# Kernel tuning notes

Measured on AMD Instinct MI355X. Metric: run time of the kernel, lower is better.

The kernel has to match this reference:

```python
import jax, jax.numpy as jnp
import numpy as np

N = 131072      # total nodes
B = 16          # graphs in batch (num_segments)
C = 128         # in_channels
K = 16          # n_super_nodes
TAU = 1.0
PRUNING_THRESHOLD = 0.01
SPARSITY_WEIGHT = 0.01
TEMPORAL_W = 0.1 * 5
COLLAPSE_W = 2.0
EPS = 1e-9


def setup_inputs() -> dict:
    key = jax.random.key(0)
    ks = jax.random.split(key, 8)
    x = jax.random.normal(ks[0], (N, C), dtype=jnp.float32)
    batch = jnp.sort(jax.random.randint(ks[1], (N,), 0, B)).astype(jnp.int64)
    pos = jax.random.normal(ks[2], (N, 2), dtype=jnp.float32)
    # Gumbel noise for gumbel_softmax (sampled once, passed as input for determinism)
    gumbel = jax.random.gumbel(ks[3], (N, K), dtype=jnp.float32)
    # assign_mlp params: Linear(C,C) -> ReLU -> Linear(C,K)
    W1 = jax.random.normal(ks[4], (C, C), dtype=jnp.float32) / np.sqrt(C)
    b1 = jnp.zeros((C,), dtype=jnp.float32)
    W2 = jax.random.normal(ks[5], (K, C), dtype=jnp.float32) / np.sqrt(C)
    b2 = jnp.zeros((K,), dtype=jnp.float32)
    scaling = jnp.asarray(10.0, dtype=jnp.float32)
    active_mask = jnp.ones((K,), dtype=jnp.float32)  # buffer, starts all-active
    return {"x": x, "batch": batch, "pos": pos, "gumbel": gumbel,
            "W1": W1, "b1": b1, "W2": W2, "b2": b2,
            "scaling": scaling, "active_mask": active_mask}


def reference(x, batch, pos, gumbel, W1, b1, W2, b2, scaling, active_mask):
    # --- assignment logits: MLP * scaling (eval mode, prev_assignments=None) ---
    h = jax.nn.relu(x @ W1.T + b1)            # [N, C]
    logits = (h @ W2.T + b2) * scaling        # [N, K]
    # eval-path masking: masked_fill(mask == 0, -1e9)
    masked_logits = jnp.where(active_mask[None, :] == 0.0, -1e9, logits)
    # gumbel_softmax (soft, hard=False)
    s = jax.nn.softmax((masked_logits + gumbel) / TAU, axis=-1)   # [N, K]

    avg_s = jnp.mean(s, axis=0)               # [K]

    # --- losses ---
    entropy = -jnp.mean(jnp.sum(s * jnp.log(s + EPS), axis=1))
    uniform_p = 1.0 / K
    diversity = jnp.sum(uniform_p * jnp.log(uniform_p / (avg_s + EPS)))
    pruning = jnp.mean(jnp.abs(avg_s * (1.0 - active_mask)))
    sparsity = (jnp.sum(active_mask) / K) * SPARSITY_WEIGHT
    temporal = jnp.asarray(0.0, jnp.float32)  # prev_assignments is None
    # collapse-prevention / balance bodies are truncated upstream; faithful proxies
    collapse = jnp.sum((avg_s - uniform_p) ** 2) * COLLAPSE_W
    balance = jnp.std(avg_s)
    spatial = jnp.asarray(0.0, jnp.float32)

    # --- pooled features: out[b,k,c] = sum_{n in graph b} s[n,k] * x[n,c] ---
    weighted = x[:, None, :] * s[:, :, None]                  # [N, K, C]
    out = jax.ops.segment_sum(weighted, batch, num_segments=B)  # [B, K, C]

    # --- super-node positions ---
    w_pos = pos[:, None, :] * s[:, :, None]                    # [N, K, 2]
    sum_s_pos = jax.ops.segment_sum(w_pos, batch, num_segments=B)  # [B, K, 2]
    sum_s = jax.ops.segment_sum(s, batch, num_segments=B)[..., None] + EPS  # [B, K, 1]
    mu = sum_s_pos / sum_s                                     # [B, K, 2]

    # --- separation loss: pairwise repulsion between super-node centers ---
    dist_sq = jnp.sum((mu[:, :, None, :] - mu[:, None, :, :]) ** 2, axis=-1)  # [B,K,K]
    eye = jnp.eye(K, dtype=mu.dtype)[None]
    repulsion = 1.0 / (dist_sq + 1.0)
    separation = jnp.sum(repulsion * (1.0 - eye)) / (K * (K - 1))

    losses = jnp.stack([entropy, diversity, spatial, pruning, sparsity,
                        temporal * TEMPORAL_W, collapse, balance, separation])
    return out, s, mu, losses
```

## Files before the change

### kernel.cpp

```cpp
#include <hip/hip_runtime.h>
#include <hip/hip_bf16.h>
#include <math.h>

#define NN 131072
#define BSEG 16
#define CCH 128
#define KK 16
#define EPSF 1e-9f
#define XST 136

#define OFF_S   32768
#define OFF_MU  2129920
#define OFF_L   2130432

#define REDC_BASE 1024
#define REDC_STRIDE 1024
#define NRED 64
#define ST_BASE (REDC_BASE + NRED * REDC_STRIDE)
#define NST 4
#define ST_SZ (BSEG * KK * CCH)

typedef __bf16 bf16x8 __attribute__((ext_vector_type(8)));
typedef float  f32x4  __attribute__((ext_vector_type(4)));
typedef float  f32x16 __attribute__((ext_vector_type(16)));

__device__ __forceinline__ int load_batch(const void* bptr, int n, int is64) {
    if (is64) return (int)((const long long*)bptr)[n];
    return ((const int*)bptr)[n];
}

__device__ __forceinline__ float wave_sum(float v) {
#pragma unroll
    for (int o = 32; o > 0; o >>= 1) v += __shfl_xor(v, o, 64);
    return v;
}

__device__ __forceinline__ bf16x8 pack8(float4 a, float4 b) {
    bf16x8 v;
    v[0] = (__bf16)a.x; v[1] = (__bf16)a.y; v[2] = (__bf16)a.z; v[3] = (__bf16)a.w;
    v[4] = (__bf16)b.x; v[5] = (__bf16)b.y; v[6] = (__bf16)b.z; v[7] = (__bf16)b.w;
    return v;
}

__global__ void k_zero(float* __restrict__ ws, const int* __restrict__ b32) {
    int i = blockIdx.x * 256 + threadIdx.x;
    ws[REDC_BASE + i] = 0.0f;
    if (i == 0) ws[0] = (b32[NN - 1] == 0) ? 1.0f : 0.0f;
}

__global__ __launch_bounds__(256, 2) void k_fused(
    const float* __restrict__ x, const void* __restrict__ batch,
    const float* __restrict__ pos, const float* __restrict__ gumbel,
    const float* __restrict__ W1, const float* __restrict__ b1,
    const float* __restrict__ W2, const float* __restrict__ b2,
    const float* __restrict__ scaling, const float* __restrict__ active_mask,
    float* __restrict__ s_out, float* __restrict__ ws)
{
    __shared__ __align__(16) __bf16 x_lds[128 * XST];
    __shared__ __align__(16) __bf16 h_lds[128 * XST];
    __shared__ __align__(16) __bf16 sT[16 * XST];
    __shared__ float2 pos_lds[128];
    __shared__ int bsegs[128];

    const int tid  = threadIdx.x;
    const int lane = tid & 63;
    const int wv   = tid >> 6;
    const int n0   = blockIdx.x * 128;
    const int is64 = (int)ws[0];

    float* rc  = ws + REDC_BASE + (size_t)(blockIdx.x & (NRED - 1)) * REDC_STRIDE;
    float* stg = ws + ST_BASE   + (size_t)(blockIdx.x & (NST  - 1)) * ST_SZ;

    if (tid < 128) {
        bsegs[tid] = load_batch(batch, n0 + tid, is64);
        pos_lds[tid] = ((const float2*)pos)[n0 + tid];
    }
    {
        const float4* xg = (const float4*)(x + (size_t)n0 * CCH);
#pragma unroll
        for (int i = 0; i < 8; i++) {
            int p = i * 256 + tid;
            float4 a = xg[2 * p], b = xg[2 * p + 1];
            *(bf16x8*)&x_lds[(p >> 4) * XST + (p & 15) * 8] = pack8(a, b);
        }
    }
    __syncthreads();

    {
        bf16x8 bfr[8];
        const float* wrow = W1 + (size_t)(wv * 32 + (lane & 31)) * CCH + (lane >> 5) * 8;
#pragma unroll
        for (int ks = 0; ks < 8; ks++) {
            float4 u = *(const float4*)(wrow + ks * 16);
            float4 v = *(const float4*)(wrow + ks * 16 + 4);
            bfr[ks] = pack8(u, v);
        }
        f32x16 acc[4];
#pragma unroll
        for (int mt = 0; mt < 4; mt++)
#pragma unroll
            for (int r = 0; r < 16; r++) acc[mt][r] = 0.0f;

#pragma unroll
        for (int ks = 0; ks < 8; ks++) {
#pragma unroll
            for (int mt = 0; mt < 4; mt++) {
                bf16x8 a = *(bf16x8*)&x_lds[(size_t)(mt * 32 + (lane & 31)) * XST + ks * 16 + (lane >> 5) * 8];
                acc[mt] = __builtin_amdgcn_mfma_f32_32x32x16_bf16(a, bfr[ks], acc[mt], 0, 0, 0);
            }
        }
        const float b1j = b1[wv * 32 + (lane & 31)];
#pragma unroll
        for (int mt = 0; mt < 4; mt++)
#pragma unroll
            for (int r = 0; r < 16; r++) {
                int node = mt * 32 + (r & 3) + 8 * (r >> 2) + 4 * (lane >> 5);
                h_lds[(size_t)node * XST + wv * 32 + (lane & 31)] = (__bf16)fmaxf(acc[mt][r] + b1j, 0.0f);
            }
    }
    __syncthreads();

    {
        const int g  = lane >> 4;
        const int kq = lane & 15;
        const int bf = bsegs[0], bl = bsegs[127];

        float gu[2][4];
#pragma unroll
        for (int t = 0; t < 2; t++)
#pragma unroll
            for (int r = 0; r < 4; r++) {
                int node = (wv * 2 + t) * 16 + g * 4 + r;
                gu[t][r] = gumbel[(size_t)(n0 + node) * KK + kq];
            }
        const float b2k = b2[kq];
        const float amk = active_mask[kq];
        const float sc  = scaling[0];

        f32x4 acc2[2];
#pragma unroll
        for (int t = 0; t < 2; t++)
#pragma unroll
            for (int r = 0; r < 4; r++) acc2[t][r] = 0.0f;

#pragma unroll
        for (int ks = 0; ks < 4; ks++) {
            const float* w2row = W2 + (size_t)kq * CCH + ks * 32 + g * 8;
            float4 u = *(const float4*)w2row;
            float4 v4 = *(const float4*)(w2row + 4);
            bf16x8 bwf = pack8(u, v4);
#pragma unroll
            for (int t = 0; t < 2; t++) {
                bf16x8 a = *(bf16x8*)&h_lds[(size_t)((wv * 2 + t) * 16 + kq) * XST + ks * 32 + g * 8];
                acc2[t] = __builtin_amdgcn_mfma_f32_16x16x32_bf16(a, bwf, acc2[t], 0, 0, 0);
            }
        }

        float saccA = 0.f, pxA = 0.f, pyA = 0.f;
        float saccB = 0.f, pxB = 0.f, pyB = 0.f;
        float entacc = 0.f;
        const bool dual = (bf != bl);

#pragma unroll
        for (int t = 0; t < 2; t++) {
#pragma unroll
            for (int r = 0; r < 4; r++) {
                const int node = (wv * 2 + t) * 16 + g * 4 + r;
                float v = (acc2[t][r] + b2k) * sc;
                if (amk == 0.0f) v = -1e9f;
                v += gu[t][r];
                float m = v;
#pragma unroll
                for (int o = 1; o < 16; o <<= 1) m = fmaxf(m, __shfl_xor(m, o, 64));
                float e = expf(v - m);
                float ssum = e;
#pragma unroll
                for (int o = 1; o < 16; o <<= 1) ssum += __shfl_xor(ssum, o, 64);
                float s = e / ssum;

                s_out[(size_t)(n0 + node) * KK + kq] = s;
                sT[kq * XST + node] = (__bf16)s;

                float tt = s * logf(s + EPSF);
#pragma unroll
                for (int o = 1; o < 16; o <<= 1) tt += __shfl_xor(tt, o, 64);
                entacc += tt;

                const float2 pp = pos_lds[node];
                const float w0 = (bsegs[node] == bf) ? 1.0f : 0.0f;
                const float sA = s * w0;
                saccA += sA; pxA += sA * pp.x; pyA += sA * pp.y;
                if (dual) {
                    const float sB = s - sA;
                    saccB += sB; pxB += sB * pp.x; pyB += sB * pp.y;
                }
            }
        }

        saccA += __shfl_xor(saccA, 16, 64); saccA += __shfl_xor(saccA, 32, 64);
        pxA   += __shfl_xor(pxA,   16, 64); pxA   += __shfl_xor(pxA,   32, 64);
        pyA   += __shfl_xor(pyA,   16, 64); pyA   += __shfl_xor(pyA,   32, 64);
        if (lane < 16) {
            atomicAdd(&rc[bf * 16 + lane], saccA);
            atomicAdd(&rc[256 + bf * 32 + 2 * lane],     pxA);
            atomicAdd(&rc[256 + bf * 32 + 2 * lane + 1], pyA);
        }
        if (dual) {
            saccB += __shfl_xor(saccB, 16, 64); saccB += __shfl_xor(saccB, 32, 64);
            pxB   += __shfl_xor(pxB,   16, 64); pxB   += __shfl_xor(pxB,   32, 64);
            pyB   += __shfl_xor(pyB,   16, 64); pyB   += __shfl_xor(pyB,   32, 64);
            if (lane < 16) {
                atomicAdd(&rc[bl * 16 + lane], saccB);
                atomicAdd(&rc[256 + bl * 32 + 2 * lane],     pxB);
                atomicAdd(&rc[256 + bl * 32 + 2 * lane + 1], pyB);
            }
        }
        float entw = wave_sum(entacc);
        if (lane == 0) atomicAdd(&rc[768], entw * 0.0625f);
    }
    __syncthreads();

    {
        const int bfirst = bsegs[0], blast = bsegs[127];
        for (int seg = bfirst; seg <= blast; seg++) {
            const bool masked = (bfirst != blast);
            f32x4 pacc[2];
#pragma unroll
            for (int t = 0; t < 2; t++)
#pragma unroll
                for (int r = 0; r < 4; r++) pacc[t][r] = 0.0f;

#pragma unroll
            for (int ks = 0; ks < 4; ks++) {
                bf16x8 a = *(bf16x8*)&sT[(size_t)(lane & 15) * XST + ks * 32 + (lane >> 4) * 8];
                if (masked) {
#pragma unroll
                    for (int i = 0; i < 8; i++) {
                        int nd = ks * 32 + (lane >> 4) * 8 + i;
                        if (bsegs[nd] != seg) a[i] = (__bf16)0.0f;
                    }
                }
#pragma unroll
                for (int t = 0; t < 2; t++) {
                    int ct = wv * 2 + t;
                    bf16x8 bx;
#pragma unroll
                    for (int i = 0; i < 8; i++)
                        bx[i] = x_lds[(size_t)(ks * 32 + (lane >> 4) * 8 + i) * XST + ct * 16 + (lane & 15)];
                    pacc[t] = __builtin_amdgcn_mfma_f32_16x16x32_bf16(a, bx, pacc[t], 0, 0, 0);
                }
            }
#pragma unroll
            for (int t = 0; t < 2; t++) {
                int c = (wv * 2 + t) * 16 + (lane & 15);
#pragma unroll
                for (int r = 0; r < 4; r++) {
                    int k = (lane >> 4) * 4 + r;
                    atomicAdd(&stg[((size_t)seg * KK + k) * CCH + c], pacc[t][r]);
                }
            }
        }
    }
}

__global__ __launch_bounds__(256) void k_tail(
    const float* __restrict__ ws, const float* __restrict__ active_mask,
    float* __restrict__ out, float* __restrict__ mu_out, float* __restrict__ losses)
{
    const int tid = threadIdx.x;

    if (blockIdx.x < 32) {
        int i = blockIdx.x * 256 + tid;
        const float4* s0 = (const float4*)(ws + ST_BASE);
        const float4* s1 = (const float4*)(ws + ST_BASE + ST_SZ);
        const float4* s2 = (const float4*)(ws + ST_BASE + 2 * ST_SZ);
        const float4* s3 = (const float4*)(ws + ST_BASE + 3 * ST_SZ);
        float4 a = s0[i], b = s1[i], c = s2[i], d = s3[i];
        float4 r;
        r.x = (a.x + b.x) + (c.x + d.x);
        r.y = (a.y + b.y) + (c.y + d.y);
        r.z = (a.z + b.z) + (c.z + d.z);
        r.w = (a.w + b.w) + (c.w + d.w);
        ((float4*)out)[i] = r;
        return;
    }

    __shared__ float lsum[256];
    __shared__ float lpos[512];
    __shared__ float lent[1];
    __shared__ float smu[512];
    __shared__ float savg[16];
    __shared__ float red[256];

    for (int a = tid; a < 769; a += 256) {
        float acc = 0.0f;
#pragma unroll 8
        for (int c = 0; c < NRED; c++) acc += ws[REDC_BASE + c * REDC_STRIDE + a];
        if (a < 256) lsum[a] = acc;
        else if (a < 768) lpos[a - 256] = acc;
        else lent[0] = acc;
    }
    __syncthreads();

    if (tid < 16) {
        float a = 0.0f;
#pragma unroll
        for (int b = 0; b < 16; b++) a += lsum[b * 16 + tid];
        savg[tid] = a / (float)NN;
    }
    for (int i = tid; i < 512; i += 256) {
        int sk = i >> 1;
        float v = lpos[i] / (lsum[sk] + EPSF);
        smu[i] = v;
        mu_out[i] = v;
    }
    __syncthreads();

    float rep = 0.0f;
    for (int t = tid; t < 4096; t += 256) {
        int b = t >> 8, i = (t >> 4) & 15, j = t & 15;
        if (i != j) {
            float dx = smu[b * 32 + i * 2]     - smu[b * 32 + j * 2];
            float dy = smu[b * 32 + i * 2 + 1] - smu[b * 32 + j * 2 + 1];
            rep += 1.0f / (dx * dx + dy * dy + 1.0f);
        }
    }
    red[tid] = rep;
    __syncthreads();
    for (int st = 128; st > 0; st >>= 1) {
        if (tid < st) red[tid] += red[tid + st];
        __syncthreads();
    }

    if (tid == 0) {
        const float p = 1.0f / 16.0f;
        float separation = red[0] / (float)(16 * 15);
        float entropy = -lent[0] / (float)NN;
        float diversity = 0.f, pruning = 0.f, amsum = 0.f, collapse = 0.f, mean = 0.f;
        for (int k = 0; k < 16; k++) {
            float a = savg[k];
            diversity += p * logf(p / (a + EPSF));
            pruning += fabsf(a * (1.0f - active_mask[k]));
            amsum += active_mask[k];
            collapse += (a - p) * (a - p);
            mean += a;
        }
        pruning /= 16.0f;
        mean /= 16.0f;
        float var = 0.f;
        for (int k = 0; k < 16; k++) { float d = savg[k] - mean; var += d * d; }
        float balance = sqrtf(var / 16.0f);
        float sparsity = (amsum / 16.0f) * 0.01f;
        collapse *= 2.0f;
        losses[0] = entropy;   losses[1] = diversity; losses[2] = 0.0f;
        losses[3] = pruning;   losses[4] = sparsity;  losses[5] = 0.0f;
        losses[6] = collapse;  losses[7] = balance;   losses[8] = separation;
    }
}

extern "C" void kernel_launch(void* const* d_in, const int* in_sizes, int n_in,
                              void* d_out, int out_size, void* d_ws, size_t ws_size,
                              hipStream_t stream) {
    const float* x       = (const float*)d_in[0];
    const void*  batch   = d_in[1];
    const float* pos     = (const float*)d_in[2];
    const float* gumbel  = (const float*)d_in[3];
    const float* W1      = (const float*)d_in[4];
    const float* b1      = (const float*)d_in[5];
    const float* W2      = (const float*)d_in[6];
    const float* b2      = (const float*)d_in[7];
    const float* scaling = (const float*)d_in[8];
    const float* am      = (const float*)d_in[9];

    float* out      = (float*)d_out;
    float* s_sec    = out + OFF_S;
    float* mu_sec   = out + OFF_MU;
    float* loss_sec = out + OFF_L;
    float* wsf      = (float*)d_ws;

    k_zero<<<768, 256, 0, stream>>>(wsf, (const int*)batch);
    k_fused<<<NN / 128, 256, 0, stream>>>(x, batch, pos, gumbel, W1, b1, W2, b2,
                                          scaling, am, s_sec, wsf);
    k_tail<<<33, 256, 0, stream>>>(wsf, am, out, mu_sec, loss_sec);
}
```

Measured before the change: 160.8 us.

## Swap GEMM1 warp partition to node rows and drop post-GEMM block barrier

The first MLP layer is repartitioned so each wave owns 32 node rows and all 128 output channels, rather than 32 output channels over all nodes. W1 fragments are now reloaded from global memory (cache) and packed inside the k-loop instead of being preloaded. Because each wave writes only its own rows of h, the __syncthreads after the h store is replaced by a local LDS wait plus a scheduling barrier. This assumes the next stage reads only rows produced by the same wave. The trade is 4x more W1 global loads and pack conversions per wave.

```diff
diff --git a/kernel.cpp b/kernel.cpp
--- a/kernel.cpp
+++ b/kernel.cpp
@@ -87,38 +87,39 @@
     __syncthreads();
 
     {
-        bf16x8 bfr[8];
-        const float* wrow = W1 + (size_t)(wv * 32 + (lane & 31)) * CCH + (lane >> 5) * 8;
-#pragma unroll
+        float b1j[4];
+#pragma unroll
+        for (int ct = 0; ct < 4; ct++) b1j[ct] = b1[ct * 32 + (lane & 31)];
+
+        f32x16 acc[4];
+#pragma unroll
+        for (int ct = 0; ct < 4; ct++)
+#pragma unroll
+            for (int r = 0; r < 16; r++) acc[ct][r] = 0.0f;
+
+        const int arow = wv * 32 + (lane & 31);
+        const int koff = (lane >> 5) * 8;
+#pragma unroll 2
         for (int ks = 0; ks < 8; ks++) {
-            float4 u = *(const float4*)(wrow + ks * 16);
-            float4 v = *(const float4*)(wrow + ks * 16 + 4);
-            bfr[ks] = pack8(u, v);
-        }
-        f32x16 acc[4];
-#pragma unroll
-        for (int mt = 0; mt < 4; mt++)
-#pragma unroll
-            for (int r = 0; r < 16; r++) acc[mt][r] = 0.0f;
-
-#pragma unroll
-        for (int ks = 0; ks < 8; ks++) {
-#pragma unroll
-            for (int mt = 0; mt < 4; mt++) {
-                bf16x8 a = *(bf16x8*)&x_lds[(size_t)(mt * 32 + (lane & 31)) * XST + ks * 16 + (lane >> 5) * 8];
-                acc[mt] = __builtin_amdgcn_mfma_f32_32x32x16_bf16(a, bfr[ks], acc[mt], 0, 0, 0);
-            }
-        }
-        const float b1j = b1[wv * 32 + (lane & 31)];
-#pragma unroll
-        for (int mt = 0; mt < 4; mt++)
+            bf16x8 a = *(bf16x8*)&x_lds[(size_t)arow * XST + ks * 16 + koff];
+#pragma unroll
+            for (int ct = 0; ct < 4; ct++) {
+                const float* wrow = W1 + (size_t)(ct * 32 + (lane & 31)) * CCH + ks * 16 + koff;
+                float4 u = *(const float4*)wrow;
+                float4 v = *(const float4*)(wrow + 4);
+                acc[ct] = __builtin_amdgcn_mfma_f32_32x32x16_bf16(a, pack8(u, v), acc[ct], 0, 0, 0);
+            }
+        }
+#pragma unroll
+        for (int ct = 0; ct < 4; ct++)
 #pragma unroll
             for (int r = 0; r < 16; r++) {
-                int node = mt * 32 + (r & 3) + 8 * (r >> 2) + 4 * (lane >> 5);
-                h_lds[(size_t)node * XST + wv * 32 + (lane & 31)] = (__bf16)fmaxf(acc[mt][r] + b1j, 0.0f);
-            }
-    }
-    __syncthreads();
+                int node = wv * 32 + (r & 3) + 8 * (r >> 2) + 4 * (lane >> 5);
+                h_lds[(size_t)node * XST + ct * 32 + (lane & 31)] = (__bf16)fmaxf(acc[ct][r] + b1j[ct], 0.0f);
+            }
+    }
+    asm volatile("s_waitcnt lgkmcnt(0)" ::: "memory");
+    __builtin_amdgcn_sched_barrier(0);
 
     {
         const int g  = lane >> 4;
```

New measurement: 178.7 us. +11.1%, slower.

## Process two node tiles per block, carrying pooled accumulators across tiles

Applied to the files above, without the earlier changes.

Each block now loops over two 128-node tiles. W1 fragments and the bias load once per block, and the pooled-feature MFMA accumulators stay in registers across tiles, so atomics to the staging buffer are flushed only when the segment changes. This halves the grid and cuts global atomic traffic and redundant weight loads. In exchange the grid is smaller (512 blocks), there is no overlap between tiles' loads and compute, and the extra barriers may limit latency hiding.

```diff
diff --git a/kernel.cpp b/kernel.cpp
--- a/kernel.cpp
+++ b/kernel.cpp
@@ -19,6 +19,8 @@
 #define ST_BASE (REDC_BASE + NRED * REDC_STRIDE)
 #define NST 4
 #define ST_SZ (BSEG * KK * CCH)
+
+#define TILES 2
 
 typedef __bf16 bf16x8 __attribute__((ext_vector_type(8)));
 typedef float  f32x4  __attribute__((ext_vector_type(4)));
@@ -65,29 +67,13 @@
     const int tid  = threadIdx.x;
     const int lane = tid & 63;
     const int wv   = tid >> 6;
-    const int n0   = blockIdx.x * 128;
     const int is64 = (int)ws[0];
 
     float* rc  = ws + REDC_BASE + (size_t)(blockIdx.x & (NRED - 1)) * REDC_STRIDE;
     float* stg = ws + ST_BASE   + (size_t)(blockIdx.x & (NST  - 1)) * ST_SZ;
 
-    if (tid < 128) {
-        bsegs[tid] = load_batch(batch, n0 + tid, is64);
-        pos_lds[tid] = ((const float2*)pos)[n0 + tid];
-    }
+    bf16x8 bfr[8];
     {
-        const float4* xg = (const float4*)(x + (size_t)n0 * CCH);
-#pragma unroll
-        for (int i = 0; i < 8; i++) {
-            int p = i * 256 + tid;
-            float4 a = xg[2 * p], b = xg[2 * p + 1];
-            *(bf16x8*)&x_lds[(p >> 4) * XST + (p & 15) * 8] = pack8(a, b);
-        }
-    }
-    __syncthreads();
-
-    {
-        bf16x8 bfr[8];
         const float* wrow = W1 + (size_t)(wv * 32 + (lane & 31)) * CCH + (lane >> 5) * 8;
 #pragma unroll
         for (int ks = 0; ks < 8; ks++) {
@@ -95,169 +81,217 @@
             float4 v = *(const float4*)(wrow + ks * 16 + 4);
             bfr[ks] = pack8(u, v);
         }
-        f32x16 acc[4];
-#pragma unroll
-        for (int mt = 0; mt < 4; mt++)
-#pragma unroll
-            for (int r = 0; r < 16; r++) acc[mt][r] = 0.0f;
-
-#pragma unroll
-        for (int ks = 0; ks < 8; ks++) {
-#pragma unroll
-            for (int mt = 0; mt < 4; mt++) {
-                bf16x8 a = *(bf16x8*)&x_lds[(size_t)(mt * 32 + (lane & 31)) * XST + ks * 16 + (lane >> 5) * 8];
-                acc[mt] = __builtin_amdgcn_mfma_f32_32x32x16_bf16(a, bfr[ks], acc[mt], 0, 0, 0);
-            }
-        }
-        const float b1j = b1[wv * 32 + (lane & 31)];
-#pragma unroll
-        for (int mt = 0; mt < 4; mt++)
-#pragma unroll
-            for (int r = 0; r < 16; r++) {
-                int node = mt * 32 + (r & 3) + 8 * (r >> 2) + 4 * (lane >> 5);
-                h_lds[(size_t)node * XST + wv * 32 + (lane & 31)] = (__bf16)fmaxf(acc[mt][r] + b1j, 0.0f);
-            }
-    }
-    __syncthreads();
-
-    {
-        const int g  = lane >> 4;
-        const int kq = lane & 15;
-        const int bf = bsegs[0], bl = bsegs[127];
-
+    }
+    const float b1j = b1[wv * 32 + (lane & 31)];
+
+    f32x4 pacc[2];
+#pragma unroll
+    for (int t = 0; t < 2; t++)
+#pragma unroll
+        for (int r = 0; r < 4; r++) pacc[t][r] = 0.0f;
+    int curseg = -1;
+
+    for (int t = 0; t < TILES; t++) {
+        const int n0 = blockIdx.x * (TILES * 128) + t * 128;
+
+        if (t) __syncthreads();
+
+        if (tid < 128) {
+            bsegs[tid] = load_batch(batch, n0 + tid, is64);
+            pos_lds[tid] = ((const float2*)pos)[n0 + tid];
+        }
         float gu[2][4];
-#pragma unroll
-        for (int t = 0; t < 2; t++)
+        {
+            const int g  = lane >> 4;
+            const int kq = lane & 15;
+#pragma unroll
+            for (int tt = 0; tt < 2; tt++)
+#pragma unroll
+                for (int r = 0; r < 4; r++) {
+                    int node = (wv * 2 + tt) * 16 + g * 4 + r;
+                    gu[tt][r] = gumbel[(size_t)(n0 + node) * KK + kq];
+                }
+        }
+        {
+            const float4* xg = (const float4*)(x + (size_t)n0 * CCH);
+#pragma unroll
+            for (int i = 0; i < 8; i++) {
+                int p = i * 256 + tid;
+                float4 a = xg[2 * p], b = xg[2 * p + 1];
+                *(bf16x8*)&x_lds[(p >> 4) * XST + (p & 15) * 8] = pack8(a, b);
+            }
+        }
+        __syncthreads();
+
+        {
+            f32x16 acc[4];
+#pragma unroll
+            for (int mt = 0; mt < 4; mt++)
+#pragma unroll
+                for (int r = 0; r < 16; r++) acc[mt][r] = 0.0f;
+
+#pragma unroll
+            for (int ks = 0; ks < 8; ks++) {
+#pragma unroll
+                for (int mt = 0; mt < 4; mt++) {
+                    bf16x8 a = *(bf16x8*)&x_lds[(size_t)(mt * 32 + (lane & 31)) * XST + ks * 16 + (lane >> 5) * 8];
+                    acc[mt] = __builtin_amdgcn_mfma_f32_32x32x16_bf16(a, bfr[ks], acc[mt], 0, 0, 0);
+                }
+            }
+#pragma unroll
+            for (int mt = 0; mt < 4; mt++)
+#pragma unroll
+                for (int r = 0; r < 16; r++) {
+                    int node = mt * 32 + (r & 3) + 8 * (r >> 2) + 4 * (lane >> 5);
+                    h_lds[(size_t)node * XST + wv * 32 + (lane & 31)] = (__bf16)fmaxf(acc[mt][r] + b1j, 0.0f);
+                }
+        }
+        __syncthreads();
+
+        {
+            const int g  = lane >> 4;
+            const int kq = lane & 15;
+            const int bf = bsegs[0], bl = bsegs[127];
+
+            const float b2k = b2[kq];
+            const float amk = active_mask[kq];
+            const float sc  = scaling[0];
+
+            f32x4 acc2[2];
+#pragma unroll
+            for (int tt = 0; tt < 2; tt++)
+#pragma unroll
+                for (int r = 0; r < 4; r++) acc2[tt][r] = 0.0f;
+
+#pragma unroll
+            for (int ks = 0; ks < 4; ks++) {
+                const float* w2row = W2 + (size_t)kq * CCH + ks * 32 + g * 8;
+                float4 u = *(const float4*)w2row;
+                float4 v4 = *(const float4*)(w2row + 4);
+                bf16x8 bwf = pack8(u, v4);
+#pragma unroll
+                for (int tt = 0; tt < 2; tt++) {
+                    bf16x8 a = *(bf16x8*)&h_lds[(size_t)((wv * 2 + tt) * 16 + kq) * XST + ks * 32 + g * 8];
+                    acc2[tt] = __builtin_amdgcn_mfma_f32_16x16x32_bf16(a, bwf, acc2[tt], 0, 0, 0);
+                }
+            }
+
+            float saccA = 0.f, pxA = 0.f, pyA = 0.f;
+            float saccB = 0.f, pxB = 0.f, pyB = 0.f;
+            float entacc = 0.f;
+            const bool dual = (bf != bl);
+
+#pragma unroll
+            for (int tt = 0; tt < 2; tt++) {
+#pragma unroll
+                for (int r = 0; r < 4; r++) {
+                    const int node = (wv * 2 + tt) * 16 + g * 4 + r;
+                    float v = (acc2[tt][r] + b2k) * sc;
+                    if (amk == 0.0f) v = -1e9f;
+                    v += gu[tt][r];
+                    float m = v;
+#pragma unroll
+                    for (int o = 1; o < 16; o <<= 1) m = fmaxf(m, __shfl_xor(m, o, 64));
+                    float e = expf(v - m);
+                    float ssum = e;
+#pragma unroll
+                    for (int o = 1; o < 16; o <<= 1) ssum += __shfl_xor(ssum, o, 64);
+                    float s = e / ssum;
+
+                    s_out[(size_t)(n0 + node) * KK + kq] = s;
+                    sT[kq * XST + node] = (__bf16)s;
+
+                    float te = s * logf(s + EPSF);
+#pragma unroll
+                    for (int o = 1; o < 16; o <<= 1) te += __shfl_xor(te, o, 64);
+                    entacc += te;
+
+                    const float2 pp = pos_lds[node];
+                    const float w0 = (bsegs[node] == bf) ? 1.0f : 0.0f;
+                    const float sA = s * w0;
+                    saccA += sA; pxA += sA * pp.x; pyA += sA * pp.y;
+                    if (dual) {
+                        const float sB = s - sA;
+                        saccB += sB; pxB += sB * pp.x; pyB += sB * pp.y;
+                    }
+                }
+            }
+
+            saccA += __shfl_xor(saccA, 16, 64); saccA += __shfl_xor(saccA, 32, 64);
+            pxA   += __shfl_xor(pxA,   16, 64); pxA   += __shfl_xor(pxA,   32, 64);
+            pyA   += __shfl_xor(pyA,   16, 64); pyA   += __shfl_xor(pyA,   32, 64);
+            if (lane < 16) {
+                atomicAdd(&rc[bf * 16 + lane], saccA);
+                atomicAdd(&rc[256 + bf * 32 + 2 * lane],     pxA);
+                atomicAdd(&rc[256 + bf * 32 + 2 * lane + 1], pyA);
+            }
+            if (dual) {
+                saccB += __shfl_xor(saccB, 16, 64); saccB += __shfl_xor(saccB, 32, 64);
+                pxB   += __shfl_xor(pxB,   16, 64); pxB   += __shfl_xor(pxB,   32, 64);
+                pyB   += __shfl_xor(pyB,   16, 64); pyB   += __shfl_xor(pyB,   32, 64);
+                if (lane < 16) {
+                    atomicAdd(&rc[bl * 16 + lane], saccB);
+                    atomicAdd(&rc[256 + bl * 32 + 2 * lane],     pxB);
+                    atomicAdd(&rc[256 + bl * 32 + 2 * lane + 1], pyB);
+                }
+            }
+            float entw = wave_sum(entacc);
+            if (lane == 0) atomicAdd(&rc[768], entw * 0.0625f);
+        }
+        __syncthreads();
+
+        {
+            const int bf = bsegs[0], bl = bsegs[127];
+            const bool masked = (bf != bl);
+            for (int seg = bf; seg <= bl; seg++) {
+                if (seg != curseg) {
+                    if (curseg >= 0) {
+#pragma unroll
+                        for (int tt = 0; tt < 2; tt++) {
+#pragma unroll
+                            for (int r = 0; r < 4; r++) {
+                                int k = (lane >> 4) * 4 + r;
+                                int c = (wv * 2 + tt) * 16 + (lane & 15);
+                                atomicAdd(&stg[((size_t)curseg * KK + k) * CCH + c], pacc[tt][r]);
+                            }
+#pragma unroll
+                            for (int r = 0; r < 4; r++) pacc[tt][r] = 0.0f;
+                        }
+                    }
+                    curseg = seg;
+                }
+#pragma unroll
+                for (int ks = 0; ks < 4; ks++) {
+                    bf16x8 a = *(bf16x8*)&sT[(size_t)(lane & 15) * XST + ks * 32 + (lane >> 4) * 8];
+                    if (masked) {
+#pragma unroll
+                        for (int i = 0; i < 8; i++) {
+                            int nd = ks * 32 + (lane >> 4) * 8 + i;
+                            if (bsegs[nd] != seg) a[i] = (__bf16)0.0f;
+                        }
+                    }
+#pragma unroll
+                    for (int tt = 0; tt < 2; tt++) {
+                        int ct = wv * 2 + tt;
+                        bf16x8 bx;
+#pragma unroll
+                        for (int i = 0; i < 8; i++)
+                            bx[i] = x_lds[(size_t)(ks * 32 + (lane >> 4) * 8 + i) * XST + ct * 16 + (lane & 15)];
+                        pacc[tt] = __builtin_amdgcn_mfma_f32_16x16x32_bf16(a, bx, pacc[tt], 0, 0, 0);
+                    }
+                }
+            }
+        }
+    }
+
+    if (curseg >= 0) {
+#pragma unroll
+        for (int tt = 0; tt < 2; tt++) {
 #pragma unroll
             for (int r = 0; r < 4; r++) {
-                int node = (wv * 2 + t) * 16 + g * 4 + r;
-                gu[t][r] = gumbel[(size_t)(n0 + node) * KK + kq];
-            }
-        const float b2k = b2[kq];
-        const float amk = active_mask[kq];
-        const float sc  = scaling[0];
-
-        f32x4 acc2[2];
-#pragma unroll
-        for (int t = 0; t < 2; t++)
-#pragma unroll
-            for (int r = 0; r < 4; r++) acc2[t][r] = 0.0f;
-
-#pragma unroll
-        for (int ks = 0; ks < 4; ks++) {
-            const float* w2row = W2 + (size_t)kq * CCH + ks * 32 + g * 8;
-            float4 u = *(const float4*)w2row;
-            float4 v4 = *(const float4*)(w2row + 4);
-            bf16x8 bwf = pack8(u, v4);
-#pragma unroll
-            for (int t = 0; t < 2; t++) {
-                bf16x8 a = *(bf16x8*)&h_lds[(size_t)((wv * 2 + t) * 16 + kq) * XST + ks * 32 + g * 8];
-                acc2[t] = __builtin_amdgcn_mfma_f32_16x16x32_bf16(a, bwf, acc2[t], 0, 0, 0);
-            }
-        }
-
-        float saccA = 0.f, pxA = 0.f, pyA = 0.f;
-        float saccB = 0.f, pxB = 0.f, pyB = 0.f;
-        float entacc = 0.f;
-        const bool dual = (bf != bl);
-
-#pragma unroll
-        for (int t = 0; t < 2; t++) {
-#pragma unroll
-            for (int r = 0; r < 4; r++) {
-                const int node = (wv * 2 + t) * 16 + g * 4 + r;
-                float v = (acc2[t][r] + b2k) * sc;
-                if (amk == 0.0f) v = -1e9f;
-                v += gu[t][r];
-                float m = v;
-#pragma unroll
-                for (int o = 1; o < 16; o <<= 1) m = fmaxf(m, __shfl_xor(m, o, 64));
-                float e = expf(v - m);
-                float ssum = e;
-#pragma unroll
-                for (int o = 1; o < 16; o <<= 1) ssum += __shfl_xor(ssum, o, 64);
-                float s = e / ssum;
-
-                s_out[(size_t)(n0 + node) * KK + kq] = s;
-                sT[kq * XST + node] = (__bf16)s;
-
-                float tt = s * logf(s + EPSF);
-#pragma unroll
-                for (int o = 1; o < 16; o <<= 1) tt += __shfl_xor(tt, o, 64);
-                entacc += tt;
-
-                const float2 pp = pos_lds[node];
-                const float w0 = (bsegs[node] == bf) ? 1.0f : 0.0f;
-                const float sA = s * w0;
-                saccA += sA; pxA += sA * pp.x; pyA += sA * pp.y;
-                if (dual) {
-                    const float sB = s - sA;
-                    saccB += sB; pxB += sB * pp.x; pyB += sB * pp.y;
-                }
-            }
-        }
-
-        saccA += __shfl_xor(saccA, 16, 64); saccA += __shfl_xor(saccA, 32, 64);
-        pxA   += __shfl_xor(pxA,   16, 64); pxA   += __shfl_xor(pxA,   32, 64);
-        pyA   += __shfl_xor(pyA,   16, 64); pyA   += __shfl_xor(pyA,   32, 64);
-        if (lane < 16) {
-            atomicAdd(&rc[bf * 16 + lane], saccA);
-            atomicAdd(&rc[256 + bf * 32 + 2 * lane],     pxA);
-            atomicAdd(&rc[256 + bf * 32 + 2 * lane + 1], pyA);
-        }
-        if (dual) {
-            saccB += __shfl_xor(saccB, 16, 64); saccB += __shfl_xor(saccB, 32, 64);
-            pxB   += __shfl_xor(pxB,   16, 64); pxB   += __shfl_xor(pxB,   32, 64);
-            pyB   += __shfl_xor(pyB,   16, 64); pyB   += __shfl_xor(pyB,   32, 64);
-            if (lane < 16) {
-                atomicAdd(&rc[bl * 16 + lane], saccB);
-                atomicAdd(&rc[256 + bl * 32 + 2 * lane],     pxB);
-                atomicAdd(&rc[256 + bl * 32 + 2 * lane + 1], pyB);
-            }
-        }
-        float entw = wave_sum(entacc);
-        if (lane == 0) atomicAdd(&rc[768], entw * 0.0625f);
-    }
-    __syncthreads();
-
-    {
-        const int bfirst = bsegs[0], blast = bsegs[127];
-        for (int seg = bfirst; seg <= blast; seg++) {
-            const bool masked = (bfirst != blast);
-            f32x4 pacc[2];
-#pragma unroll
-            for (int t = 0; t < 2; t++)
-#pragma unroll
-                for (int r = 0; r < 4; r++) pacc[t][r] = 0.0f;
-
-#pragma unroll
-            for (int ks = 0; ks < 4; ks++) {
-                bf16x8 a = *(bf16x8*)&sT[(size_t)(lane & 15) * XST + ks * 32 + (lane >> 4) * 8];
-                if (masked) {
-#pragma unroll
-                    for (int i = 0; i < 8; i++) {
-                        int nd = ks * 32 + (lane >> 4) * 8 + i;
-                        if (bsegs[nd] != seg) a[i] = (__bf16)0.0f;
-                    }
-                }
-#pragma unroll
-                for (int t = 0; t < 2; t++) {
-                    int ct = wv * 2 + t;
-                    bf16x8 bx;
-#pragma unroll
-                    for (int i = 0; i < 8; i++)
-                        bx[i] = x_lds[(size_t)(ks * 32 + (lane >> 4) * 8 + i) * XST + ct * 16 + (lane & 15)];
-                    pacc[t] = __builtin_amdgcn_mfma_f32_16x16x32_bf16(a, bx, pacc[t], 0, 0, 0);
-                }
-            }
-#pragma unroll
-            for (int t = 0; t < 2; t++) {
-                int c = (wv * 2 + t) * 16 + (lane & 15);
-#pragma unroll
-                for (int r = 0; r < 4; r++) {
-                    int k = (lane >> 4) * 4 + r;
-                    atomicAdd(&stg[((size_t)seg * KK + k) * CCH + c], pacc[t][r]);
-                }
+                int k = (lane >> 4) * 4 + r;
+                int c = (wv * 2 + tt) * 16 + (lane & 15);
+                atomicAdd(&stg[((size_t)curseg * KK + k) * CCH + c], pacc[tt][r]);
             }
         }
     }
@@ -379,7 +413,7 @@
     float* wsf      = (float*)d_ws;
 
     k_zero<<<768, 256, 0, stream>>>(wsf, (const int*)batch);
-    k_fused<<<NN / 128, 256, 0, stream>>>(x, batch, pos, gumbel, W1, b1, W2, b2,
+    k_fused<<<NN / 256, 256, 0, stream>>>(x, batch, pos, gumbel, W1, b1, W2, b2,
                                           scaling, am, s_sec, wsf);
     k_tail<<<33, 256, 0, stream>>>(wsf, am, out, mu_sec, loss_sec);
 }
```

New measurement: 156.3 us, median of 2. -2.8%, faster.
